# Optimization experiments

Hardware: AMD Instinct MI355X
Metric: run time of the kernel (lower is better)

## Reference

```python
import jax, jax.numpy as jnp
import numpy as np

EPS = 1e-05
SINKHORN_ITERS = 20


def sinkhorn_knopp(M):
    M = jnp.exp(M)
    def body(_, M):
        M = M / (M.sum(axis=1, keepdims=True) + EPS)
        M = M / (M.sum(axis=0, keepdims=True) + EPS)
        return M
    return jax.lax.fori_loop(0, SINKHORN_ITERS, body, M)


def setup_inputs() -> dict:
    key = jax.random.key(0)
    k1, k2 = jax.random.split(key)
    B, n, C = 4096, 4, 4096
    alpha_init = 0.01
    return {
        "x_expanded": jax.random.normal(k1, (B, n, C), dtype=jnp.float32),
        "rmsnorm_weight": jnp.ones((C,), dtype=jnp.float32),
        "H_pre": jnp.zeros((n,), dtype=jnp.float32),
        "H_post": jnp.zeros((n,), dtype=jnp.float32),
        "H_res": alpha_init * jax.random.normal(k2, (n, n), dtype=jnp.float32),
    }


def reference(x_expanded, rmsnorm_weight, H_pre, H_post, H_res):
    B, n, C = x_expanded.shape
    H_pre_act = jax.nn.sigmoid(H_pre)            # (n,)
    H_post_act = 2.0 * jax.nn.sigmoid(H_post)    # (n,)
    M = sinkhorn_knopp(H_res)                    # (n, n) doubly-stochastic-ish

    # aggregate across expansion dim: (B, C)
    x_agg = jnp.einsum('i,bic->bc', H_pre_act, x_expanded)
    # RMSNorm over C
    rms = jnp.sqrt(jnp.mean(x_agg * x_agg, axis=-1, keepdims=True) + EPS)
    x_normed = x_agg / rms * rmsnorm_weight      # (B, C)

    y_dist = H_post_act[None, :, None] * x_normed[:, None, :]  # (B, n, C)
    x_mixed = jnp.einsum('ij,bjc->bic', M, x_expanded)          # (B, n, C)
    return x_mixed + y_dist
```

## Files before the change

kernel.cpp:

```cpp
#include <hip/hip_runtime.h>
#include <math.h>

#define EPSF 1e-5f
#define SINKHORN_ITERS 20
#define C_DIM 4096
#define N_DIM 4

__global__ void prep_kernel(const float* __restrict__ H_pre,
                            const float* __restrict__ H_post,
                            const float* __restrict__ H_res,
                            float* __restrict__ params) {
    if (threadIdx.x != 0 || blockIdx.x != 0) return;
    float M[4][4];
    for (int i = 0; i < 4; ++i)
        for (int j = 0; j < 4; ++j)
            M[i][j] = expf(H_res[i * 4 + j]);
    for (int it = 0; it < SINKHORN_ITERS; ++it) {
        for (int i = 0; i < 4; ++i) {
            float s = M[i][0] + M[i][1] + M[i][2] + M[i][3] + EPSF;
            M[i][0] /= s; M[i][1] /= s; M[i][2] /= s; M[i][3] /= s;
        }
        for (int j = 0; j < 4; ++j) {
            float s = M[0][j] + M[1][j] + M[2][j] + M[3][j] + EPSF;
            M[0][j] /= s; M[1][j] /= s; M[2][j] /= s; M[3][j] /= s;
        }
    }
    for (int i = 0; i < 4; ++i) {
        params[i]     = 1.0f / (1.0f + expf(-H_pre[i]));
        params[4 + i] = 2.0f / (1.0f + expf(-H_post[i]));
    }
    for (int i = 0; i < 4; ++i)
        for (int j = 0; j < 4; ++j)
            params[8 + i * 4 + j] = M[i][j];
}

__global__ __launch_bounds__(1024)
void fused_kernel(const float* __restrict__ x,
                  const float* __restrict__ w,
                  const float* __restrict__ params,
                  float* __restrict__ out) {
    const int b = blockIdx.x;
    const int t = threadIdx.x;

    __shared__ float s_params[24];
    __shared__ float s_partial[16];
    __shared__ float s_inv;

    if (t < 24) s_params[t] = params[t];
    __syncthreads();

    const size_t row_base = (size_t)b * (N_DIM * C_DIM);
    const int c0 = t * 4;

    float4 x0 = *reinterpret_cast<const float4*>(x + row_base + 0 * C_DIM + c0);
    float4 x1 = *reinterpret_cast<const float4*>(x + row_base + 1 * C_DIM + c0);
    float4 x2 = *reinterpret_cast<const float4*>(x + row_base + 2 * C_DIM + c0);
    float4 x3 = *reinterpret_cast<const float4*>(x + row_base + 3 * C_DIM + c0);
    float4 w4 = *reinterpret_cast<const float4*>(w + c0);

    const float p0 = s_params[0], p1 = s_params[1], p2 = s_params[2], p3 = s_params[3];

    float4 agg;
    agg.x = p0 * x0.x + p1 * x1.x + p2 * x2.x + p3 * x3.x;
    agg.y = p0 * x0.y + p1 * x1.y + p2 * x2.y + p3 * x3.y;
    agg.z = p0 * x0.z + p1 * x1.z + p2 * x2.z + p3 * x3.z;
    agg.w = p0 * x0.w + p1 * x1.w + p2 * x2.w + p3 * x3.w;

    float ss = agg.x * agg.x + agg.y * agg.y + agg.z * agg.z + agg.w * agg.w;

    for (int off = 32; off > 0; off >>= 1)
        ss += __shfl_down(ss, off, 64);
    const int wid = t >> 6;
    const int lane = t & 63;
    if (lane == 0) s_partial[wid] = ss;
    __syncthreads();
    if (t == 0) {
        float tot = 0.0f;
        for (int k = 0; k < 16; ++k) tot += s_partial[k];
        s_inv = 1.0f / sqrtf(tot * (1.0f / (float)C_DIM) + EPSF);
    }
    __syncthreads();
    const float inv = s_inv;

    float4 nw;
    nw.x = agg.x * inv * w4.x;
    nw.y = agg.y * inv * w4.y;
    nw.z = agg.z * inv * w4.z;
    nw.w = agg.w * inv * w4.w;

    #pragma unroll
    for (int i = 0; i < 4; ++i) {
        const float m0 = s_params[8 + i * 4 + 0];
        const float m1 = s_params[8 + i * 4 + 1];
        const float m2 = s_params[8 + i * 4 + 2];
        const float m3 = s_params[8 + i * 4 + 3];
        const float po = s_params[4 + i];
        float4 o;
        o.x = m0 * x0.x + m1 * x1.x + m2 * x2.x + m3 * x3.x + po * nw.x;
        o.y = m0 * x0.y + m1 * x1.y + m2 * x2.y + m3 * x3.y + po * nw.y;
        o.z = m0 * x0.z + m1 * x1.z + m2 * x2.z + m3 * x3.z + po * nw.z;
        o.w = m0 * x0.w + m1 * x1.w + m2 * x2.w + m3 * x3.w + po * nw.w;
        *reinterpret_cast<float4*>(out + row_base + i * C_DIM + c0) = o;
    }
}

extern "C" void kernel_launch(void* const* d_in, const int* in_sizes, int n_in,
                              void* d_out, int out_size, void* d_ws, size_t ws_size,
                              hipStream_t stream) {
    const float* x      = (const float*)d_in[0];
    const float* w      = (const float*)d_in[1];
    const float* H_pre  = (const float*)d_in[2];
    const float* H_post = (const float*)d_in[3];
    const float* H_res  = (const float*)d_in[4];
    float* out    = (float*)d_out;
    float* params = (float*)d_ws;

    const int B = in_sizes[0] / (N_DIM * C_DIM);

    prep_kernel<<<1, 64, 0, stream>>>(H_pre, H_post, H_res, params);
    fused_kernel<<<B, 1024, 0, stream>>>(x, w, params, out);
}
```

Before: 122.9 us.

## Use 256-thread blocks with 16 nontemporal vector loads per thread and one barrier

Each block shrinks from 1024 to 256 threads, and each thread now handles four strided float4 chunks per row, so there are 16 loads in flight per thread. Loads and stores use nontemporal builtins to avoid polluting the cache. The RMS reduction drops from two barriers to one, with every thread summing four shared partials, and the params are read straight from global memory instead of staged through LDS. The cost is higher register pressure from holding 16 float4 values, which could limit occupancy.

Result: faster. 113.9 us (-7.3%).

```diff
diff --git a/kernel.cpp b/kernel.cpp
--- a/kernel.cpp
+++ b/kernel.cpp
@@ -5,6 +5,8 @@
 #define SINKHORN_ITERS 20
 #define C_DIM 4096
 #define N_DIM 4
+
+typedef __attribute__((ext_vector_type(4))) float fx4;
 
 __global__ void prep_kernel(const float* __restrict__ H_pre,
                             const float* __restrict__ H_post,
@@ -34,7 +36,7 @@
             params[8 + i * 4 + j] = M[i][j];
 }
 
-__global__ __launch_bounds__(1024)
+__global__ __launch_bounds__(256, 4)
 void fused_kernel(const float* __restrict__ x,
                   const float* __restrict__ w,
                   const float* __restrict__ params,
@@ -42,65 +44,52 @@
     const int b = blockIdx.x;
     const int t = threadIdx.x;
 
-    __shared__ float s_params[24];
-    __shared__ float s_partial[16];
-    __shared__ float s_inv;
+    const float p0 = params[0], p1 = params[1], p2 = params[2], p3 = params[3];
 
-    if (t < 24) s_params[t] = params[t];
-    __syncthreads();
-
-    const size_t row_base = (size_t)b * (N_DIM * C_DIM);
+    const size_t base = (size_t)b * (N_DIM * C_DIM);
     const int c0 = t * 4;
 
-    float4 x0 = *reinterpret_cast<const float4*>(x + row_base + 0 * C_DIM + c0);
-    float4 x1 = *reinterpret_cast<const float4*>(x + row_base + 1 * C_DIM + c0);
-    float4 x2 = *reinterpret_cast<const float4*>(x + row_base + 2 * C_DIM + c0);
-    float4 x3 = *reinterpret_cast<const float4*>(x + row_base + 3 * C_DIM + c0);
-    float4 w4 = *reinterpret_cast<const float4*>(w + c0);
+    fx4 xv[4][4];
+    #pragma unroll
+    for (int i = 0; i < 4; ++i)
+        #pragma unroll
+        for (int k = 0; k < 4; ++k)
+            xv[i][k] = __builtin_nontemporal_load(
+                reinterpret_cast<const fx4*>(x + base + i * C_DIM + k * 1024 + c0));
 
-    const float p0 = s_params[0], p1 = s_params[1], p2 = s_params[2], p3 = s_params[3];
+    float ss = 0.0f;
+    #pragma unroll
+    for (int k = 0; k < 4; ++k) {
+        fx4 a = p0 * xv[0][k] + p1 * xv[1][k] + p2 * xv[2][k] + p3 * xv[3][k];
+        ss += a.x * a.x + a.y * a.y + a.z * a.z + a.w * a.w;
+    }
 
-    float4 agg;
-    agg.x = p0 * x0.x + p1 * x1.x + p2 * x2.x + p3 * x3.x;
-    agg.y = p0 * x0.y + p1 * x1.y + p2 * x2.y + p3 * x3.y;
-    agg.z = p0 * x0.z + p1 * x1.z + p2 * x2.z + p3 * x3.z;
-    agg.w = p0 * x0.w + p1 * x1.w + p2 * x2.w + p3 * x3.w;
-
-    float ss = agg.x * agg.x + agg.y * agg.y + agg.z * agg.z + agg.w * agg.w;
-
+    #pragma unroll
     for (int off = 32; off > 0; off >>= 1)
         ss += __shfl_down(ss, off, 64);
-    const int wid = t >> 6;
-    const int lane = t & 63;
-    if (lane == 0) s_partial[wid] = ss;
+    __shared__ float sp[4];
+    if ((t & 63) == 0) sp[t >> 6] = ss;
     __syncthreads();
-    if (t == 0) {
-        float tot = 0.0f;
-        for (int k = 0; k < 16; ++k) tot += s_partial[k];
-        s_inv = 1.0f / sqrtf(tot * (1.0f / (float)C_DIM) + EPSF);
-    }
-    __syncthreads();
-    const float inv = s_inv;
-
-    float4 nw;
-    nw.x = agg.x * inv * w4.x;
-    nw.y = agg.y * inv * w4.y;
-    nw.z = agg.z * inv * w4.z;
-    nw.w = agg.w * inv * w4.w;
+    const float tot = sp[0] + sp[1] + sp[2] + sp[3];
+    const float inv = 1.0f / sqrtf(tot * (1.0f / (float)C_DIM) + EPSF);
 
     #pragma unroll
-    for (int i = 0; i < 4; ++i) {
-        const float m0 = s_params[8 + i * 4 + 0];
-        const float m1 = s_params[8 + i * 4 + 1];
-        const float m2 = s_params[8 + i * 4 + 2];
-        const float m3 = s_params[8 + i * 4 + 3];
-        const float po = s_params[4 + i];
-        float4 o;
-        o.x = m0 * x0.x + m1 * x1.x + m2 * x2.x + m3 * x3.x + po * nw.x;
-        o.y = m0 * x0.y + m1 * x1.y + m2 * x2.y + m3 * x3.y + po * nw.y;
-        o.z = m0 * x0.z + m1 * x1.z + m2 * x2.z + m3 * x3.z + po * nw.z;
-        o.w = m0 * x0.w + m1 * x1.w + m2 * x2.w + m3 * x3.w + po * nw.w;
-        *reinterpret_cast<float4*>(out + row_base + i * C_DIM + c0) = o;
+    for (int k = 0; k < 4; ++k) {
+        fx4 wv = *reinterpret_cast<const fx4*>(w + k * 1024 + c0);
+        fx4 a = p0 * xv[0][k] + p1 * xv[1][k] + p2 * xv[2][k] + p3 * xv[3][k];
+        fx4 nw = a * inv * wv;
+        #pragma unroll
+        for (int i = 0; i < 4; ++i) {
+            const float m0 = params[8 + i * 4 + 0];
+            const float m1 = params[8 + i * 4 + 1];
+            const float m2 = params[8 + i * 4 + 2];
+            const float m3 = params[8 + i * 4 + 3];
+            const float po = params[4 + i];
+            fx4 o = m0 * xv[0][k] + m1 * xv[1][k] + m2 * xv[2][k] + m3 * xv[3][k]
+                  + po * nw;
+            __builtin_nontemporal_store(
+                o, reinterpret_cast<fx4*>(out + base + i * C_DIM + k * 1024 + c0));
+        }
     }
 }
 
@@ -118,5 +107,5 @@
     const int B = in_sizes[0] / (N_DIM * C_DIM);
 
     prep_kernel<<<1, 64, 0, stream>>>(H_pre, H_post, H_res, params);
-    fused_kernel<<<B, 1024, 0, stream>>>(x, w, params, out);
+    fused_kernel<<<B, 256, 0, stream>>>(x, w, params, out);
 }
```
